# Kernel optimization log

Measured on AMD Instinct MI355X. Metric: run time of the kernel, lower is better.

## Reference

```python
import jax, jax.numpy as jnp
import numpy as np

DIM = 192
BASE = 10000.0
DIM_T = DIM // 3
DIM_Y = DIM // 3
DIM_X = DIM - DIM_T - DIM_Y


def _inv_freq(d):
    return 1.0 / (BASE ** (jnp.arange(0, d, 2, dtype=jnp.float32) / d))


def setup_inputs() -> dict:
    key = jax.random.key(0)
    x = jax.random.normal(key, (1, DIM), dtype=jnp.float32)
    return {
        "x": x,
        "inv_freq_t": _inv_freq(DIM_T),
        "inv_freq_y": _inv_freq(DIM_Y),
        "inv_freq_x": _inv_freq(DIM_X),
        "height": 64,
        "width": 64,
        "num_frames": 32,
    }


def _build(inv_freq_t, inv_freq_y, inv_freq_x, height, width, num_frames, dtype):
    pos_t = jnp.arange(num_frames, dtype=jnp.float32)
    pos_y = jnp.arange(height, dtype=jnp.float32)
    pos_x = jnp.arange(width, dtype=jnp.float32)
    # outer products then duplicate along feature dim ([T, dim_t] etc.)
    ft = jnp.concatenate([pos_t[:, None] * inv_freq_t[None, :]] * 2, axis=-1)
    fy = jnp.concatenate([pos_y[:, None] * inv_freq_y[None, :]] * 2, axis=-1)
    fx = jnp.concatenate([pos_x[:, None] * inv_freq_x[None, :]] * 2, axis=-1)
    T, H, W = num_frames, height, width

    def tile3(at, ay, ax):
        # broadcast [T,dt],[H,dy],[W,dx] -> [T*H*W, dim]
        bt = jnp.broadcast_to(at[:, None, None, :], (T, H, W, DIM_T))
        by = jnp.broadcast_to(ay[None, :, None, :], (T, H, W, DIM_Y))
        bx = jnp.broadcast_to(ax[None, None, :, :], (T, H, W, DIM_X))
        return jnp.concatenate([bt, by, bx], axis=-1).reshape(T * H * W, DIM)

    cos = tile3(jnp.cos(ft), jnp.cos(fy), jnp.cos(fx)).astype(dtype)
    sin = tile3(jnp.sin(ft), jnp.sin(fy), jnp.sin(fx)).astype(dtype)
    return cos, sin


def reference(x, inv_freq_t, inv_freq_y, inv_freq_x, height, width, num_frames):
    return _build(inv_freq_t, inv_freq_y, inv_freq_x, height, width, num_frames, x.dtype)
```

## Files before the change

kernel.cpp:

```cpp
#include <hip/hip_runtime.h>


#define T_FRAMES 32
#define HGT 64
#define WID 64
#define NPOS (T_FRAMES * HGT * WID)
#define DIMC 192
#define TAB_FLOATS 10240

__global__ void mrope_build_tables(const float* __restrict__ ift,
                                   const float* __restrict__ ify,
                                   const float* __restrict__ ifx,
                                   float* __restrict__ ws) {
    int i = blockIdx.x * blockDim.x + threadIdx.x;
    float* wc = ws;
    float* wn = ws + TAB_FLOATS;
    if (i < 1024) {
        int p = i >> 5, j = i & 31;
        float s, c;
        sincosf((float)p * ift[j], &s, &c);
        int b = p * 64 + j;
        wc[b] = c; wc[b + 32] = c;
        wn[b] = s; wn[b + 32] = s;
    } else if (i < 3072) {
        int k = i - 1024; int p = k >> 5, j = k & 31;
        float s, c;
        sincosf((float)p * ify[j], &s, &c);
        int b = 2048 + p * 64 + j;
        wc[b] = c; wc[b + 32] = c;
        wn[b] = s; wn[b + 32] = s;
    } else if (i < 5120) {
        int k = i - 3072; int p = k >> 5, j = k & 31;
        float s, c;
        sincosf((float)p * ifx[j], &s, &c);
        int b = 6144 + p * 64 + j;
        wc[b] = c; wc[b + 32] = c;
        wn[b] = s; wn[b + 32] = s;
    }
}

__global__ void mrope_write(const float* __restrict__ ws, float* __restrict__ out) {
    const int totalv = NPOS * DIMC / 4;
    const float4* __restrict__ wc = (const float4*)ws;
    const float4* __restrict__ wn = (const float4*)(ws + TAB_FLOATS);
    float4* __restrict__ oc = (float4*)out;
    float4* __restrict__ os = (float4*)(out + (size_t)NPOS * DIMC);
    int stride = gridDim.x * blockDim.x;
    for (int v = blockIdx.x * blockDim.x + threadIdx.x; v < totalv; v += stride) {
        int p  = v / 48;
        int dv = v - p * 48;
        int seg = dv >> 4;
        int t = p >> 12;
        int y = (p >> 6) & 63;
        int x = p & 63;
        int c, base;
        if (seg == 0)      { c = t; base = 0;    }
        else if (seg == 1) { c = y; base = 512;  }
        else               { c = x; base = 1536; }
        int idx = base + c * 16 + (dv & 15);
        oc[v] = wc[idx];
        os[v] = wn[idx];
    }
}

__global__ void mrope_direct(const float* __restrict__ ift,
                             const float* __restrict__ ify,
                             const float* __restrict__ ifx,
                             float* __restrict__ out) {
    const long long total = (long long)NPOS * DIMC;
    long long stride = (long long)gridDim.x * blockDim.x;
    for (long long e = blockIdx.x * (long long)blockDim.x + threadIdx.x; e < total; e += stride) {
        int p = (int)(e / DIMC);
        int d = (int)(e - (long long)p * DIMC);
        int t = p >> 12, y = (p >> 6) & 63, x = p & 63;
        float coord; const float* invf; int j;
        if (d < 64)       { coord = (float)t; invf = ift; j = d & 31; }
        else if (d < 128) { coord = (float)y; invf = ify; j = (d - 64) & 31; }
        else              { coord = (float)x; invf = ifx; j = (d - 128) & 31; }
        float s, c;
        sincosf(coord * invf[j], &s, &c);
        out[e] = c;
        out[e + (long long)NPOS * DIMC] = s;
    }
}

extern "C" void kernel_launch(void* const* d_in, const int* in_sizes, int n_in,
                              void* d_out, int out_size, void* d_ws, size_t ws_size,
                              hipStream_t stream) {
    const float* ift = (const float*)d_in[1];
    const float* ify = (const float*)d_in[2];
    const float* ifx = (const float*)d_in[3];
    float* out = (float*)d_out;

    if (ws_size >= 2 * TAB_FLOATS * sizeof(float)) {
        float* ws = (float*)d_ws;
        mrope_build_tables<<<20, 256, 0, stream>>>(ift, ify, ifx, ws);
        mrope_write<<<2048, 256, 0, stream>>>(ws, out);
    } else {
        mrope_direct<<<2048, 256, 0, stream>>>(ift, ify, ifx, out);
    }
}
```

Measured before the change: 41.13 us.

## Fuse table build into single kernel with fast intrinsics and nontemporal stores

Replaces the two-kernel scheme (build a sin/cos table in workspace, then copy it out) with one kernel that computes cos/sin inline from the inverse-frequency vectors, using four-wide vector loads. It uses the fast __cosf/__sinf intrinsics and nontemporal stores. The aim is to drop the second launch and the dependent table reads, since the kernel is bound by its output writes. In exchange it recomputes transcendentals per element and uses lower-accuracy intrinsics, whose error grows with larger arguments (up to about 63 radians).

```diff
diff --git a/kernel.cpp b/kernel.cpp
--- a/kernel.cpp
+++ b/kernel.cpp
@@ -6,81 +6,35 @@
 #define WID 64
 #define NPOS (T_FRAMES * HGT * WID)
 #define DIMC 192
-#define TAB_FLOATS 10240
 
-__global__ void mrope_build_tables(const float* __restrict__ ift,
-                                   const float* __restrict__ ify,
-                                   const float* __restrict__ ifx,
-                                   float* __restrict__ ws) {
-    int i = blockIdx.x * blockDim.x + threadIdx.x;
-    float* wc = ws;
-    float* wn = ws + TAB_FLOATS;
-    if (i < 1024) {
-        int p = i >> 5, j = i & 31;
-        float s, c;
-        sincosf((float)p * ift[j], &s, &c);
-        int b = p * 64 + j;
-        wc[b] = c; wc[b + 32] = c;
-        wn[b] = s; wn[b + 32] = s;
-    } else if (i < 3072) {
-        int k = i - 1024; int p = k >> 5, j = k & 31;
-        float s, c;
-        sincosf((float)p * ify[j], &s, &c);
-        int b = 2048 + p * 64 + j;
-        wc[b] = c; wc[b + 32] = c;
-        wn[b] = s; wn[b + 32] = s;
-    } else if (i < 5120) {
-        int k = i - 3072; int p = k >> 5, j = k & 31;
-        float s, c;
-        sincosf((float)p * ifx[j], &s, &c);
-        int b = 6144 + p * 64 + j;
-        wc[b] = c; wc[b + 32] = c;
-        wn[b] = s; wn[b + 32] = s;
-    }
-}
+typedef float f4v __attribute__((ext_vector_type(4)));
 
-__global__ void mrope_write(const float* __restrict__ ws, float* __restrict__ out) {
+__global__ __launch_bounds__(256) void mrope_fused(
+    const float* __restrict__ ift,
+    const float* __restrict__ ify,
+    const float* __restrict__ ifx,
+    float* __restrict__ out)
+{
     const int totalv = NPOS * DIMC / 4;
-    const float4* __restrict__ wc = (const float4*)ws;
-    const float4* __restrict__ wn = (const float4*)(ws + TAB_FLOATS);
-    float4* __restrict__ oc = (float4*)out;
-    float4* __restrict__ os = (float4*)(out + (size_t)NPOS * DIMC);
-    int stride = gridDim.x * blockDim.x;
+    f4v* __restrict__ oc = (f4v*)out;
+    f4v* __restrict__ os = (f4v*)(out + (size_t)NPOS * DIMC);
+    const int stride = gridDim.x * blockDim.x;
     for (int v = blockIdx.x * blockDim.x + threadIdx.x; v < totalv; v += stride) {
         int p  = v / 48;
         int dv = v - p * 48;
         int seg = dv >> 4;
-        int t = p >> 12;
-        int y = (p >> 6) & 63;
-        int x = p & 63;
-        int c, base;
-        if (seg == 0)      { c = t; base = 0;    }
-        else if (seg == 1) { c = y; base = 512;  }
-        else               { c = x; base = 1536; }
-        int idx = base + c * 16 + (dv & 15);
-        oc[v] = wc[idx];
-        os[v] = wn[idx];
-    }
-}
-
-__global__ void mrope_direct(const float* __restrict__ ift,
-                             const float* __restrict__ ify,
-                             const float* __restrict__ ifx,
-                             float* __restrict__ out) {
-    const long long total = (long long)NPOS * DIMC;
-    long long stride = (long long)gridDim.x * blockDim.x;
-    for (long long e = blockIdx.x * (long long)blockDim.x + threadIdx.x; e < total; e += stride) {
-        int p = (int)(e / DIMC);
-        int d = (int)(e - (long long)p * DIMC);
-        int t = p >> 12, y = (p >> 6) & 63, x = p & 63;
-        float coord; const float* invf; int j;
-        if (d < 64)       { coord = (float)t; invf = ift; j = d & 31; }
-        else if (d < 128) { coord = (float)y; invf = ify; j = (d - 64) & 31; }
-        else              { coord = (float)x; invf = ifx; j = (d - 128) & 31; }
-        float s, c;
-        sincosf(coord * invf[j], &s, &c);
-        out[e] = c;
-        out[e + (long long)NPOS * DIMC] = s;
+        int coord; const float* invf;
+        if (seg == 0)      { coord = p >> 12;       invf = ift; }
+        else if (seg == 1) { coord = (p >> 6) & 63; invf = ify; }
+        else               { coord = p & 63;        invf = ifx; }
+        f4v fr = ((const f4v*)invf)[dv & 7];
+        float cf = (float)coord;
+        float a0 = cf * fr.x, a1 = cf * fr.y, a2 = cf * fr.z, a3 = cf * fr.w;
+        f4v vc, vs;
+        vc.x = __cosf(a0); vc.y = __cosf(a1); vc.z = __cosf(a2); vc.w = __cosf(a3);
+        vs.x = __sinf(a0); vs.y = __sinf(a1); vs.z = __sinf(a2); vs.w = __sinf(a3);
+        __builtin_nontemporal_store(vc, &oc[v]);
+        __builtin_nontemporal_store(vs, &os[v]);
     }
 }
 
@@ -90,13 +44,5 @@
     const float* ift = (const float*)d_in[1];
     const float* ify = (const float*)d_in[2];
     const float* ifx = (const float*)d_in[3];
-    float* out = (float*)d_out;
-
-    if (ws_size >= 2 * TAB_FLOATS * sizeof(float)) {
-        float* ws = (float*)d_ws;
-        mrope_build_tables<<<20, 256, 0, stream>>>(ift, ify, ifx, ws);
-        mrope_write<<<2048, 256, 0, stream>>>(ws, out);
-    } else {
-        mrope_direct<<<2048, 256, 0, stream>>>(ift, ify, ifx, out);
-    }
+    mrope_fused<<<2048, 256, 0, stream>>>(ift, ify, ifx, (float*)d_out);
 }
```

Result: faster. 40.15 us (-2.4%).
